# Kernel optimization log

Hardware: AMD Instinct MI355X
Metric: run time of the kernel (lower is better)

The kernel has to match this reference:

```python
import jax, jax.numpy as jnp
import numpy as np

N = 50000      # nodes
E = 600000     # edges
D = 128        # dim_h == num_features
G = 512        # graphs in batch
BN_EPS = 1e-5


def _w(k, shape, fan_in):
    return jax.random.normal(k, shape, jnp.float32) * np.float32(1.0 / np.sqrt(fan_in))


def setup_inputs() -> dict:
    key = jax.random.key(0)
    ks = jax.random.split(key, 16)
    return {
        "x": jax.random.normal(ks[0], (N, D), jnp.float32),
        "edge_index": jax.random.randint(ks[1], (2, E), 0, N, jnp.int64),
        "batch": jnp.sort(jax.random.randint(ks[2], (N,), 0, G, jnp.int64)),
        # GINConv 1 MLP: Linear -> BN -> ReLU -> Linear -> ReLU
        "c1_W1": _w(ks[3], (D, D), D), "c1_b1": jnp.zeros((D,), jnp.float32),
        "c1_g": jnp.ones((D,), jnp.float32), "c1_be": jnp.zeros((D,), jnp.float32),
        "c1_W2": _w(ks[4], (D, D), D), "c1_b2": jnp.zeros((D,), jnp.float32),
        # GINConv 2 MLP
        "c2_W1": _w(ks[5], (D, D), D), "c2_b1": jnp.zeros((D,), jnp.float32),
        "c2_g": jnp.ones((D,), jnp.float32), "c2_be": jnp.zeros((D,), jnp.float32),
        "c2_W2": _w(ks[6], (D, D), D), "c2_b2": jnp.zeros((D,), jnp.float32),
        # readout MLP
        "lin1_W": _w(ks[7], (4 * D, 4 * D), 4 * D), "lin1_b": jnp.zeros((4 * D,), jnp.float32),
        "lin2_W": _w(ks[8], (4 * D, 1), 4 * D), "lin2_b": jnp.zeros((1,), jnp.float32),
    }


def _gin_conv(x, src, dst, W1, b1, g, be, W2, b2):
    # sum aggregation of neighbor messages (PyG GINConv, eps=0)
    agg = jax.ops.segment_sum(x[src], dst, num_segments=x.shape[0])
    h = (agg + x) @ W1 + b1
    # BatchNorm1d, training mode (biased batch stats over nodes)
    mu = h.mean(axis=0)
    var = h.var(axis=0)
    h = jax.nn.relu(g * (h - mu) * jax.lax.rsqrt(var + BN_EPS) + be)
    return jax.nn.relu(h @ W2 + b2)


def _pool(h, batch):
    add = jax.ops.segment_sum(h, batch, num_segments=G)
    mx = jax.ops.segment_max(h, batch, num_segments=G)
    mx = jnp.where(jnp.isfinite(mx), mx, 0.0)  # empty segments -> 0
    return add, mx


def reference(x, edge_index, batch,
              c1_W1, c1_b1, c1_g, c1_be, c1_W2, c1_b2,
              c2_W1, c2_b1, c2_g, c2_be, c2_W2, c2_b2,
              lin1_W, lin1_b, lin2_W, lin2_b):
    src, dst = edge_index[0], edge_index[1]
    h1 = _gin_conv(x, src, dst, c1_W1, c1_b1, c1_g, c1_be, c1_W2, c1_b2)
    h2 = _gin_conv(h1, src, dst, c2_W1, c2_b1, c2_g, c2_be, c2_W2, c2_b2)
    a1, m1 = _pool(h1, batch)
    a2, m2 = _pool(h2, batch)
    h = jnp.concatenate([a1, a2, m1, m2], axis=1)  # [G, 4D]
    h = jax.nn.relu(h @ lin1_W + lin1_b)
    h = h @ lin2_W + lin2_b  # [G, 1]
    return jax.nn.sigmoid(h), h
```

## Files before the change

### kernel.cpp

```cpp
#include <hip/hip_runtime.h>

#define D 128
#define GNUM 512

typedef _Float16 f16;
typedef _Float16 f16x2 __attribute__((ext_vector_type(2)));
typedef _Float16 f16x8 __attribute__((ext_vector_type(8)));
typedef float f32x4 __attribute__((ext_vector_type(4)));

__global__ void deg_kernel(const int* __restrict__ ei, int* __restrict__ deg,
                           int nE) {
  int e = blockIdx.x * blockDim.x + threadIdx.x;
  if (e < nE) atomicAdd(&deg[ei[nE + e]], 1);
}

__global__ __launch_bounds__(256) void partial_kernel(
    const int* __restrict__ deg, int* __restrict__ partials, int n) {
  __shared__ int sh[256];
  const int t = threadIdx.x;
  const int i = blockIdx.x * 512 + t * 2;
  int s = 0;
  if (i < n) s += deg[i];
  if (i + 1 < n) s += deg[i + 1];
  sh[t] = s;
  __syncthreads();
#pragma unroll
  for (int off = 128; off > 0; off >>= 1) {
    if (t < off) sh[t] += sh[t + off];
    __syncthreads();
  }
  if (t == 0) partials[blockIdx.x] = sh[0];
}

__global__ __launch_bounds__(128) void scanp_kernel(
    int* __restrict__ partials, int nP, int* __restrict__ rowptr, int n,
    int nE) {
  __shared__ int sh[128];
  const int t = threadIdx.x;
  const int v = (t < nP) ? partials[t] : 0;
  sh[t] = v;
  __syncthreads();
#pragma unroll
  for (int off = 1; off < 128; off <<= 1) {
    int u = (t >= off) ? sh[t - off] : 0;
    __syncthreads();
    sh[t] += u;
    __syncthreads();
  }
  if (t < nP) partials[t] = sh[t] - v;
  if (t == 0) rowptr[n] = nE;
}

__global__ __launch_bounds__(256) void emit_kernel(
    const int* __restrict__ deg, const int* __restrict__ partials,
    int* __restrict__ rowptr, int* __restrict__ cursor, int n) {
  __shared__ int sh[256];
  const int t = threadIdx.x;
  const int i = blockIdx.x * 512 + t * 2;
  const int d0 = (i < n) ? deg[i] : 0;
  const int d1 = (i + 1 < n) ? deg[i + 1] : 0;
  const int s = d0 + d1;
  sh[t] = s;
  __syncthreads();
#pragma unroll
  for (int off = 1; off < 256; off <<= 1) {
    int u = (t >= off) ? sh[t - off] : 0;
    __syncthreads();
    sh[t] += u;
    __syncthreads();
  }
  int base = partials[blockIdx.x] + sh[t] - s;
  if (i < n) {
    rowptr[i] = base;
    cursor[i] = base;
    base += d0;
  }
  if (i + 1 < n) {
    rowptr[i + 1] = base;
    cursor[i + 1] = base;
  }
}

__global__ void fill_kernel(const int* __restrict__ ei, int* __restrict__ cursor,
                            int* __restrict__ csr, int nE) {
  int e = blockIdx.x * blockDim.x + threadIdx.x;
  if (e < nE) {
    int d = ei[nE + e];
    int pos = atomicAdd(&cursor[d], 1);
    csr[pos] = ei[e];
  }
}

__global__ __launch_bounds__(256) void prep_kernel(
    const float* __restrict__ x, f16* __restrict__ x16, int n4,
    const float* __restrict__ W0, const float* __restrict__ W1,
    const float* __restrict__ W2, const float* __restrict__ W3,
    f16* __restrict__ wt, const int* __restrict__ batch,
    int* __restrict__ gstart, int n, int nxblk) {
  const int b = blockIdx.x;
  if (b < nxblk) {
    int i = b * 256 + threadIdx.x;
    if (i < n4) {
      float4 v = ((const float4*)x)[i];
      union { f16 h[4]; uint2 u; } p;
      p.h[0] = (f16)v.x; p.h[1] = (f16)v.y;
      p.h[2] = (f16)v.z; p.h[3] = (f16)v.w;
      ((uint2*)x16)[i] = p.u;
    }
  } else if (b < nxblk + 256) {
    int idx = (b - nxblk) * 256 + threadIdx.x;
    int wsel = idx >> 14;
    int rem = idx & 16383;
    int col = rem >> 7, k = rem & 127;
    const float* W = (wsel == 0) ? W0 : (wsel == 1) ? W1
                                      : (wsel == 2) ? W2 : W3;
    wt[idx] = (f16)W[k * D + col];
  } else {
    int g = (b - nxblk - 256) * 256 + threadIdx.x;
    if (g > GNUM) return;
    if (g == GNUM) { gstart[g] = n; return; }
    int lo = 0, hi = n;
    while (lo < hi) {
      int mid = (lo + hi) >> 1;
      if (batch[mid] < g) lo = mid + 1; else hi = mid;
    }
    gstart[g] = lo;
  }
}

__global__ __launch_bounds__(256) void aggw_kernel(
    const f16* __restrict__ feat, const int* __restrict__ rowptr,
    const int* __restrict__ csr, f16* __restrict__ out, int n) {
  const int row = blockIdx.x * 4 + (threadIdx.x >> 6);
  const int l = threadIdx.x & 63;
  if (row >= n) return;
  const int c = l * 2;
  float a0, a1;
  {
    f16x2 v = *(const f16x2*)(feat + (size_t)row * D + c);
    a0 = (float)v[0]; a1 = (float)v[1];
  }
  const int beg = rowptr[row], end = rowptr[row + 1];
  int i = beg;
  for (; i + 3 < end; i += 4) {
    int s0 = csr[i], s1 = csr[i + 1], s2 = csr[i + 2], s3 = csr[i + 3];
    f16x2 v0 = *(const f16x2*)(feat + (size_t)s0 * D + c);
    f16x2 v1 = *(const f16x2*)(feat + (size_t)s1 * D + c);
    f16x2 v2 = *(const f16x2*)(feat + (size_t)s2 * D + c);
    f16x2 v3 = *(const f16x2*)(feat + (size_t)s3 * D + c);
    a0 += (float)v0[0] + (float)v1[0] + (float)v2[0] + (float)v3[0];
    a1 += (float)v0[1] + (float)v1[1] + (float)v2[1] + (float)v3[1];
  }
  for (; i < end; i++) {
    f16x2 v = *(const f16x2*)(feat + (size_t)csr[i] * D + c);
    a0 += (float)v[0];
    a1 += (float)v[1];
  }
  f16x2 o;
  o[0] = (f16)a0;
  o[1] = (f16)a1;
  *(f16x2*)(out + (size_t)row * D + c) = o;
}

template <int BN, int OUT>
__global__ __launch_bounds__(64) void gemm16_kernel(
    const f16* __restrict__ A, const float* __restrict__ ss,
    const f16* __restrict__ WT, const float* __restrict__ bias,
    f16* __restrict__ C, float* __restrict__ pstat, int n) {
  const int l = threadIdx.x;
  const int rw0 = blockIdx.x * 32;
  const int lr = l & 15;
  const int lq = l >> 4;
  const int lk = lq * 8;

  f32x4 acc[2][8];
#pragma unroll
  for (int m = 0; m < 2; m++)
#pragma unroll
    for (int nt = 0; nt < 8; nt++) acc[m][nt] = (f32x4)0.f;

#pragma unroll
  for (int s = 0; s < 4; s++) {
    const int k = s * 32 + lk;
    f16x8 af[2];
#pragma unroll
    for (int m = 0; m < 2; m++) {
      int row = rw0 + m * 16 + lr;
      f16x8 v = (f16x8)(f16)0.f;
      if (row < n) v = *(const f16x8*)(A + (size_t)row * D + k);
      if (BN) {
        float4 c0 = *(const float4*)(ss + k);
        float4 c1 = *(const float4*)(ss + k + 4);
        float4 h0 = *(const float4*)(ss + 128 + k);
        float4 h1 = *(const float4*)(ss + 128 + k + 4);
        f16x8 r;
        r[0] = (f16)fmaxf(0.f, fmaf((float)v[0], c0.x, h0.x));
        r[1] = (f16)fmaxf(0.f, fmaf((float)v[1], c0.y, h0.y));
        r[2] = (f16)fmaxf(0.f, fmaf((float)v[2], c0.z, h0.z));
        r[3] = (f16)fmaxf(0.f, fmaf((float)v[3], c0.w, h0.w));
        r[4] = (f16)fmaxf(0.f, fmaf((float)v[4], c1.x, h1.x));
        r[5] = (f16)fmaxf(0.f, fmaf((float)v[5], c1.y, h1.y));
        r[6] = (f16)fmaxf(0.f, fmaf((float)v[6], c1.z, h1.z));
        r[7] = (f16)fmaxf(0.f, fmaf((float)v[7], c1.w, h1.w));
        af[m] = r;
      } else {
        af[m] = v;
      }
    }
    f16x8 bf[8];
#pragma unroll
    for (int nt = 0; nt < 8; nt++)
      bf[nt] = *(const f16x8*)(WT + (size_t)(nt * 16 + lr) * D + k);
#pragma unroll
    for (int m = 0; m < 2; m++)
#pragma unroll
      for (int nt = 0; nt < 8; nt++)
        acc[m][nt] = __builtin_amdgcn_mfma_f32_16x16x32_f16(af[m], bf[nt],
                                                            acc[m][nt], 0, 0, 0);
  }

  if constexpr (OUT == 0) {
    float ts[8], tq[8];
#pragma unroll
    for (int nt = 0; nt < 8; nt++) { ts[nt] = 0.f; tq[nt] = 0.f; }
#pragma unroll
    for (int m = 0; m < 2; m++)
#pragma unroll
      for (int r = 0; r < 4; r++) {
        int row = rw0 + m * 16 + lq * 4 + r;
        if (row < n) {
#pragma unroll
          for (int nt = 0; nt < 8; nt++) {
            float v = acc[m][nt][r] + bias[nt * 16 + lr];
            C[(size_t)row * D + nt * 16 + lr] = (f16)v;
            ts[nt] += v;
            tq[nt] = fmaf(v, v, tq[nt]);
          }
        }
      }
#pragma unroll
    for (int nt = 0; nt < 8; nt++) {
      ts[nt] += __shfl_xor(ts[nt], 16); ts[nt] += __shfl_xor(ts[nt], 32);
      tq[nt] += __shfl_xor(tq[nt], 16); tq[nt] += __shfl_xor(tq[nt], 32);
    }
    if (l < 16) {
      float* ps = pstat + (size_t)blockIdx.x * 256;
#pragma unroll
      for (int nt = 0; nt < 8; nt++) {
        ps[nt * 16 + l] = ts[nt];
        ps[128 + nt * 16 + l] = tq[nt];
      }
    }
  } else {
#pragma unroll
    for (int m = 0; m < 2; m++)
#pragma unroll
      for (int r = 0; r < 4; r++) {
        int row = rw0 + m * 16 + lq * 4 + r;
        if (row < n) {
#pragma unroll
          for (int nt = 0; nt < 8; nt++) {
            float v = fmaxf(0.f, acc[m][nt][r] + bias[nt * 16 + lr]);
            C[(size_t)row * D + nt * 16 + lr] = (f16)v;
          }
        }
      }
  }
}

__global__ __launch_bounds__(256) void statreduce_kernel(
    const float* __restrict__ pstat, float* __restrict__ pstat2, int nB) {
  int c = threadIdx.x;
  float s = 0.f;
  for (int b = blockIdx.x; b < nB; b += 32)
    s += pstat[(size_t)b * 256 + c];
  pstat2[(size_t)blockIdx.x * 256 + c] = s;
}

__global__ void bnstats_kernel(const float* __restrict__ pstat2,
                               const float* __restrict__ g,
                               const float* __restrict__ be,
                               float* __restrict__ ss, int n) {
  int c = threadIdx.x;
  float s = 0.f, sq = 0.f;
#pragma unroll
  for (int i = 0; i < 32; i++) {
    s += pstat2[i * 256 + c];
    sq += pstat2[i * 256 + 128 + c];
  }
  float inv_n = 1.0f / (float)n;
  float mean = s * inv_n;
  float var = sq * inv_n - mean * mean;
  float scale = g[c] * rsqrtf(var + 1e-5f);
  ss[c] = scale;
  ss[128 + c] = be[c] - mean * scale;
}

__global__ __launch_bounds__(512) void poolout_kernel(
    const f16* __restrict__ h1, const f16* __restrict__ h2,
    const int* __restrict__ gstart, const float* __restrict__ W1,
    const float* __restrict__ b1, const float* __restrict__ W2,
    const float* __restrict__ b2, float* __restrict__ out) {
  __shared__ float prow[2][512];
  __shared__ float shred[8][2];
  const int t = threadIdx.x;
  const int g0 = blockIdx.x * 2;
  {
    const int sub = t >> 8;
    const int src = (t >> 7) & 1;
    const int c = t & 127;
    const f16* hp = src ? h2 : h1;
    const int r0 = gstart[g0 + sub], r1 = gstart[g0 + sub + 1];
    float s = 0.f, m = 0.f;
    int r = r0;
    for (; r + 1 < r1; r += 2) {
      float a = (float)hp[(size_t)r * D + c];
      float b = (float)hp[(size_t)(r + 1) * D + c];
      s += a + b;
      m = fmaxf(m, fmaxf(a, b));
    }
    if (r < r1) {
      float a = (float)hp[(size_t)r * D + c];
      s += a;
      m = fmaxf(m, a);
    }
    prow[sub][src * 128 + c] = s;
    prow[sub][256 + src * 128 + c] = m;
  }
  __syncthreads();
  float a00 = 0.f, a01 = 0.f, a10 = 0.f, a11 = 0.f;
  for (int k = 0; k < 512; k += 2) {
    float w0 = W1[(size_t)k * 512 + t];
    float w1 = W1[(size_t)(k + 1) * 512 + t];
    a00 = fmaf(prow[0][k], w0, a00);
    a01 = fmaf(prow[0][k + 1], w1, a01);
    a10 = fmaf(prow[1][k], w0, a10);
    a11 = fmaf(prow[1][k + 1], w1, a11);
  }
  const float bj = b1[t];
  const float w2 = W2[t];
  float acc0 = fmaxf(0.f, a00 + a01 + bj) * w2;
  float acc1 = fmaxf(0.f, a10 + a11 + bj) * w2;
  const int w = t >> 6, l = t & 63;
#pragma unroll
  for (int off = 32; off > 0; off >>= 1) {
    acc0 += __shfl_down(acc0, off);
    acc1 += __shfl_down(acc1, off);
  }
  if (l == 0) {
    shred[w][0] = acc0;
    shred[w][1] = acc1;
  }
  __syncthreads();
  if (t < 2) {
    float s = 0.f;
#pragma unroll
    for (int i = 0; i < 8; i++) s += shred[i][t];
    float h = s + b2[0];
    out[g0 + t] = 1.0f / (1.0f + expf(-h));
    out[GNUM + g0 + t] = h;
  }
}

extern "C" void kernel_launch(void* const* d_in, const int* in_sizes, int n_in,
                              void* d_out, int out_size, void* d_ws,
                              size_t ws_size, hipStream_t stream) {
  const float* x = (const float*)d_in[0];
  const int* ei = (const int*)d_in[1];
  const int* batch = (const int*)d_in[2];
  const float* c1_W1 = (const float*)d_in[3];
  const float* c1_b1 = (const float*)d_in[4];
  const float* c1_g  = (const float*)d_in[5];
  const float* c1_be = (const float*)d_in[6];
  const float* c1_W2 = (const float*)d_in[7];
  const float* c1_b2 = (const float*)d_in[8];
  const float* c2_W1 = (const float*)d_in[9];
  const float* c2_b1 = (const float*)d_in[10];
  const float* c2_g  = (const float*)d_in[11];
  const float* c2_be = (const float*)d_in[12];
  const float* c2_W2 = (const float*)d_in[13];
  const float* c2_b2 = (const float*)d_in[14];
  const float* lin1_W = (const float*)d_in[15];
  const float* lin1_b = (const float*)d_in[16];
  const float* lin2_W = (const float*)d_in[17];
  const float* lin2_b = (const float*)d_in[18];

  const int n = in_sizes[0] / D;
  const int nE = in_sizes[1] / 2;

  char* p = (char*)d_ws;
  auto take = [&](size_t bytes) {
    char* r = p;
    p += (bytes + 255) & ~(size_t)255;
    return r;
  };
  f16*   hpre   = (f16*)take((size_t)n * D * 2);
  f16*   aggt   = (f16*)take((size_t)n * D * 2);
  f16*   h1     = (f16*)take((size_t)n * D * 2);
  f16*   wt     = (f16*)take(4 * 16384 * 2);
  int*   deg    = (int*)take((size_t)n * 4);
  float* ssbuf  = (float*)take(256 * 4);
  int*   gstart = (int*)take((GNUM + 1) * 4);
  int* rowptr   = (int*)take((size_t)(n + 1) * 4);
  int* cursor   = (int*)take((size_t)(n + 1) * 4);
  int* partials = (int*)take(128 * 4);
  int* csr      = (int*)take((size_t)nE * 4);
  const int nB = (n + 31) / 32;
  float* pstat  = (float*)take((size_t)nB * 256 * 4);
  float* pstat2 = (float*)take(32 * 256 * 4);

  const int edge_grid = (nE + 255) / 256;
  const int aggw_grid = (n + 3) / 4;
  const int nP = (n + 511) / 512;
  const int n4 = n * D / 4;
  const int nxblk = (n4 + 255) / 256;
  const int prep_grid = nxblk + 256 + 3;

  hipMemsetAsync(deg, 0, (size_t)n * sizeof(int), stream);
  deg_kernel<<<edge_grid, 256, 0, stream>>>(ei, deg, nE);
  partial_kernel<<<nP, 256, 0, stream>>>(deg, partials, n);
  scanp_kernel<<<1, 128, 0, stream>>>(partials, nP, rowptr, n, nE);
  emit_kernel<<<nP, 256, 0, stream>>>(deg, partials, rowptr, cursor, n);
  fill_kernel<<<edge_grid, 256, 0, stream>>>(ei, cursor, csr, nE);
  prep_kernel<<<prep_grid, 256, 0, stream>>>(x, h1, n4, c1_W1, c1_W2, c2_W1,
                                             c2_W2, wt, batch, gstart, n,
                                             nxblk);

  aggw_kernel<<<aggw_grid, 256, 0, stream>>>(h1, rowptr, csr, aggt, n);
  gemm16_kernel<0, 0><<<nB, 64, 0, stream>>>(aggt, nullptr, wt, c1_b1, hpre,
                                             pstat, n);
  statreduce_kernel<<<32, 256, 0, stream>>>(pstat, pstat2, nB);
  bnstats_kernel<<<1, 128, 0, stream>>>(pstat2, c1_g, c1_be, ssbuf, n);
  gemm16_kernel<1, 1><<<nB, 64, 0, stream>>>(hpre, ssbuf, wt + 16384, c1_b2,
                                             h1, nullptr, n);

  aggw_kernel<<<aggw_grid, 256, 0, stream>>>(h1, rowptr, csr, aggt, n);
  gemm16_kernel<0, 0><<<nB, 64, 0, stream>>>(aggt, nullptr, wt + 32768, c2_b1,
                                             hpre, pstat, n);
  statreduce_kernel<<<32, 256, 0, stream>>>(pstat, pstat2, nB);
  bnstats_kernel<<<1, 128, 0, stream>>>(pstat2, c2_g, c2_be, ssbuf, n);
  gemm16_kernel<1, 1><<<nB, 64, 0, stream>>>(hpre, ssbuf, wt + 49152, c2_b2,
                                             aggt, nullptr, n);

  poolout_kernel<<<GNUM / 2, 512, 0, stream>>>(h1, aggt, gstart, lin1_W,
                                               lin1_b, lin2_W, lin2_b,
                                               (float*)d_out);
}
```

Measured before the change: 271.3 us.

## Slice neighbor aggregation by column block with persistent grid and split edges

Replaces the one-wave-per-row aggregation with a persistent grid-stride kernel. Each block handles one 32-column slice of the features, and the two half-waves split a row's edges between them, combining partial sums with a cross-lane shuffle. The intent is a smaller working set per slice for better cache locality and more edge-level parallelism. In exchange, each lane now loads 2 bytes instead of 4, every edge index is re-read once per slice, and a shuffle-reduce is added per row.

```diff
diff --git a/kernel.cpp b/kernel.cpp
--- a/kernel.cpp
+++ b/kernel.cpp
@@ -128,38 +128,39 @@
   }
 }
 
-__global__ __launch_bounds__(256) void aggw_kernel(
+__global__ __launch_bounds__(256) void aggs_kernel(
     const f16* __restrict__ feat, const int* __restrict__ rowptr,
     const int* __restrict__ csr, f16* __restrict__ out, int n) {
-  const int row = blockIdx.x * 4 + (threadIdx.x >> 6);
+  const int slice = blockIdx.x & 3;
+  const int w = threadIdx.x >> 6;
   const int l = threadIdx.x & 63;
-  if (row >= n) return;
-  const int c = l * 2;
-  float a0, a1;
-  {
-    f16x2 v = *(const f16x2*)(feat + (size_t)row * D + c);
-    a0 = (float)v[0]; a1 = (float)v[1];
-  }
-  const int beg = rowptr[row], end = rowptr[row + 1];
-  int i = beg;
-  for (; i + 3 < end; i += 4) {
-    int s0 = csr[i], s1 = csr[i + 1], s2 = csr[i + 2], s3 = csr[i + 3];
-    f16x2 v0 = *(const f16x2*)(feat + (size_t)s0 * D + c);
-    f16x2 v1 = *(const f16x2*)(feat + (size_t)s1 * D + c);
-    f16x2 v2 = *(const f16x2*)(feat + (size_t)s2 * D + c);
-    f16x2 v3 = *(const f16x2*)(feat + (size_t)s3 * D + c);
-    a0 += (float)v0[0] + (float)v1[0] + (float)v2[0] + (float)v3[0];
-    a1 += (float)v0[1] + (float)v1[1] + (float)v2[1] + (float)v3[1];
-  }
-  for (; i < end; i++) {
-    f16x2 v = *(const f16x2*)(feat + (size_t)csr[i] * D + c);
-    a0 += (float)v[0];
-    a1 += (float)v[1];
-  }
-  f16x2 o;
-  o[0] = (f16)a0;
-  o[1] = (f16)a1;
-  *(f16x2*)(out + (size_t)row * D + c) = o;
+  const int half = l >> 5;
+  const int cbase = slice * 32 + (l & 31);
+  const int row0 = (blockIdx.x >> 2) * 4 + w;
+  const int rstride = gridDim.x;
+
+  for (int row = row0; row < n; row += rstride) {
+    float a = (half == 0) ? (float)feat[(size_t)row * D + cbase] : 0.f;
+    const int beg = rowptr[row], end = rowptr[row + 1];
+    int i = beg;
+    float b = 0.f;
+    for (; i + 3 < end; i += 4) {
+      int s0 = csr[i + half];
+      int s1 = csr[i + 2 + half];
+      a += (float)feat[(size_t)s0 * D + cbase];
+      b += (float)feat[(size_t)s1 * D + cbase];
+    }
+    if (i + 1 < end) {
+      int s0 = csr[i + half];
+      a += (float)feat[(size_t)s0 * D + cbase];
+      i += 2;
+    }
+    if (i < end && half == 0)
+      b += (float)feat[(size_t)csr[i] * D + cbase];
+    a += b;
+    a += __shfl_xor(a, 32);
+    if (half == 0) out[(size_t)row * D + cbase] = (f16)a;
+  }
 }
 
 template <int BN, int OUT>
@@ -410,7 +411,7 @@
   float* pstat2 = (float*)take(32 * 256 * 4);
 
   const int edge_grid = (nE + 255) / 256;
-  const int aggw_grid = (n + 3) / 4;
+  const int aggs_grid = 2048;
   const int nP = (n + 511) / 512;
   const int n4 = n * D / 4;
   const int nxblk = (n4 + 255) / 256;
@@ -426,7 +427,7 @@
                                              c2_W2, wt, batch, gstart, n,
                                              nxblk);
 
-  aggw_kernel<<<aggw_grid, 256, 0, stream>>>(h1, rowptr, csr, aggt, n);
+  aggs_kernel<<<aggs_grid, 256, 0, stream>>>(h1, rowptr, csr, aggt, n);
   gemm16_kernel<0, 0><<<nB, 64, 0, stream>>>(aggt, nullptr, wt, c1_b1, hpre,
                                              pstat, n);
   statreduce_kernel<<<32, 256, 0, stream>>>(pstat, pstat2, nB);
@@ -434,7 +435,7 @@
   gemm16_kernel<1, 1><<<nB, 64, 0, stream>>>(hpre, ssbuf, wt + 16384, c1_b2,
                                              h1, nullptr, n);
 
-  aggw_kernel<<<aggw_grid, 256, 0, stream>>>(h1, rowptr, csr, aggt, n);
+  aggs_kernel<<<aggs_grid, 256, 0, stream>>>(h1, rowptr, csr, aggt, n);
   gemm16_kernel<0, 0><<<nB, 64, 0, stream>>>(aggt, nullptr, wt + 32768, c2_b1,
                                              hpre, pstat, n);
   statreduce_kernel<<<32, 256, 0, stream>>>(pstat, pstat2, nB);
```

Result: slower. 370.7 us (+36.6%).
